# Optimization experiments

Hardware: AMD Instinct MI355X
Metric: run time of the kernel (lower is better)

## Reference

```python
import jax, jax.numpy as jnp
import numpy as np

B, S, D, H = 2, 2048, 1024, 16
HD = D // H  # head_dim = 64


def setup_inputs() -> dict:
    key = jax.random.key(0)
    ks = jax.random.split(key, 11)
    init = 1.0 / np.sqrt(D)
    inp = {
        "query": jax.random.normal(ks[0], (B, S, D), jnp.float32),
        "key": jax.random.normal(ks[1], (B, S, D), jnp.float32),
        "value": jax.random.normal(ks[2], (B, S, D), jnp.float32),
        "Wq": jax.random.uniform(ks[3], (D, D), jnp.float32, -init, init),
        "bq": jax.random.uniform(ks[4], (D,), jnp.float32, -init, init),
        "Wk": jax.random.uniform(ks[5], (D, D), jnp.float32, -init, init),
        "bk": jax.random.uniform(ks[6], (D,), jnp.float32, -init, init),
        "Wv": jax.random.uniform(ks[7], (D, D), jnp.float32, -init, init),
        "bv": jax.random.uniform(ks[8], (D,), jnp.float32, -init, init),
        "Wo": jax.random.uniform(ks[9], (D, D), jnp.float32, -init, init),
        "bo": jax.random.uniform(ks[10], (D,), jnp.float32, -init, init),
    }
    return inp


def reference(query, key, value, Wq, bq, Wk, bk, Wv, bv, Wo, bo):
    # Linear projections (torch Linear: x @ W.T + b)
    q = query @ Wq.T + bq  # [B,S,D]
    k = key @ Wk.T + bk
    v = value @ Wv.T + bv
    # split heads -> [B,H,S,HD]
    q = q.reshape(B, S, H, HD).transpose(0, 2, 1, 3)
    k = k.reshape(B, S, H, HD).transpose(0, 2, 1, 3)
    v = v.reshape(B, S, H, HD).transpose(0, 2, 1, 3)
    # NOTE: original code divides by scale = head_dim**-0.5, i.e. multiplies
    # scores by sqrt(head_dim). Reproduced faithfully.
    scale = HD ** (-0.5)
    scores = jnp.einsum("bhqd,bhkd->bhqk", q, k) / scale  # [B,H,S,S]
    attn = jax.nn.softmax(scores, axis=-1)
    x = jnp.einsum("bhqk,bhkd->bhqd", attn, v)  # [B,H,S,HD]
    x = x.transpose(0, 2, 1, 3).reshape(B, S, D)
    return x @ Wo.T + bo
```

## Files before the change

### kernel.cpp

```cpp
#include <hip/hip_runtime.h>
#include <stdint.h>
#include <stddef.h>

#define SCALE_LOG2E 11.541560327111707f
#define E8 4194304
#define M1 1048576
#define NROW 65536

typedef __attribute__((ext_vector_type(8))) _Float16 f16x8;
typedef __attribute__((ext_vector_type(4))) _Float16 f16x4;
typedef __attribute__((ext_vector_type(4))) float f32x4;

#if __has_builtin(__builtin_amdgcn_exp2f)
#define EXP2F(x) __builtin_amdgcn_exp2f(x)
#else
#define EXP2F(x) exp2f(x)
#endif

__device__ __forceinline__ f32x4 mfma_f16(f16x8 a, f16x8 b, f32x4 c) {
  return __builtin_amdgcn_mfma_f32_16x16x32_f16(a, b, c, 0, 0, 0);
}

__device__ __forceinline__ f32x4 mfma16_f16(f16x4 a, f16x4 b, f32x4 c) {
  return __builtin_amdgcn_mfma_f32_16x16x16f16(a, b, c, 0, 0, 0);
}

__device__ __forceinline__ void async16(const void* g, void* lds) {
  __builtin_amdgcn_global_load_lds(
      (const __attribute__((address_space(1))) unsigned int*)g,
      (__attribute__((address_space(3))) unsigned int*)lds, 16, 0, 0);
}

__global__ void prep_all(const float* __restrict__ q, const float* __restrict__ k,
                         const float* __restrict__ v,
                         const float* __restrict__ wq, const float* __restrict__ wk,
                         const float* __restrict__ wv, const float* __restrict__ wo,
                         _Float16* __restrict__ Xf, _Float16* __restrict__ Wf) {
  const int gid = blockIdx.x;
  const float* src;
  _Float16* dst;
  int i;
  if (gid < 12288) {
    const int z = gid >> 12;
    src = (z == 0) ? q : (z == 1) ? k : v;
    dst = Xf + (size_t)z * E8;
    i = (gid & 4095) * 256 + threadIdx.x;
  } else {
    const int g2 = gid - 12288;
    const int z = g2 >> 10;
    src = (z == 0) ? wq : (z == 1) ? wk : (z == 2) ? wv : wo;
    dst = Wf + (size_t)z * M1;
    i = (g2 & 1023) * 256 + threadIdx.x;
  }
  float4 x = ((const float4*)src)[i];
  f16x4 h = {(_Float16)x.x, (_Float16)x.y, (_Float16)x.z, (_Float16)x.w};
  ((f16x4*)dst)[i] = h;
}

__global__ __launch_bounds__(256, 3) void gemm_qkv(
    const _Float16* __restrict__ Xf,
    const _Float16* __restrict__ Wf,
    const float* __restrict__ bq, const float* __restrict__ bk,
    const float* __restrict__ bv,
    _Float16* __restrict__ Of)
{
  __shared__ _Float16 SMEM[16384];
  _Float16* LA = SMEM;
  _Float16* LB = SMEM + 8192;
  const int z = blockIdx.z;
  const int tid = threadIdx.x;
  const int lane = tid & 63;
  const int wv = tid >> 6;
  const int wm = wv >> 1, wn = wv & 1;
  const int rl = lane & 15, qd = lane >> 4;
  const int m0 = blockIdx.y * 128, n0 = blockIdx.x * 128;

  const _Float16* A0 = Xf + (size_t)z * E8;
  const _Float16* W0 = Wf + (size_t)z * M1;
  const float* bias = (z == 0) ? bq : (z == 1) ? bk : bv;

  f32x4 acc[4][4];
#pragma unroll
  for (int i = 0; i < 4; i++)
#pragma unroll
    for (int j = 0; j < 4; j++) acc[i][j] = f32x4{0.f, 0.f, 0.f, 0.f};

  const int srow = wv * 32 + (lane >> 2);
  const int scol = (lane & 3) * 8;

  auto stage = [&](int k0, int buf) {
    const _Float16* ga = A0 + (size_t)(m0 + srow) * 1024 + k0 + scol;
    async16(ga, &LA[buf * 4096 + wv * 1024]);
    async16(ga + 16 * 1024, &LA[buf * 4096 + wv * 1024 + 512]);
    const _Float16* gb = W0 + (size_t)(n0 + srow) * 1024 + k0 + scol;
    async16(gb, &LB[buf * 4096 + wv * 1024]);
    async16(gb + 16 * 1024, &LB[buf * 4096 + wv * 1024 + 512]);
  };

  stage(0, 0);
  for (int t = 0; t < 32; t++) {
    const int buf = t & 1;
    __syncthreads();
    if (t + 1 < 32) stage((t + 1) * 32, buf ^ 1);
    f16x8 af[4], bfr[4];
#pragma unroll
    for (int i = 0; i < 4; i++) af[i] = *(const f16x8*)&LA[buf * 4096 + (wm * 64 + i * 16 + rl) * 32 + qd * 8];
#pragma unroll
    for (int j = 0; j < 4; j++) bfr[j] = *(const f16x8*)&LB[buf * 4096 + (wn * 64 + j * 16 + rl) * 32 + qd * 8];
#pragma unroll
    for (int i = 0; i < 4; i++)
#pragma unroll
      for (int j = 0; j < 4; j++) acc[i][j] = mfma_f16(af[i], bfr[j], acc[i][j]);
  }

  if (z == 2) {
#pragma unroll
    for (int j = 0; j < 4; j++) {
      const int nn = n0 + wn * 64 + j * 16 + rl;
      const float bj = bias[nn];
      const int hh = nn >> 6, e = nn & 63;
#pragma unroll
      for (int i = 0; i < 4; i++) {
        const int mm = m0 + wm * 64 + i * 16 + qd * 4;
        const int b = mm >> 11, s = mm & 2047;
        f16x4 pk = {(_Float16)(acc[i][j][0] + bj), (_Float16)(acc[i][j][1] + bj),
                    (_Float16)(acc[i][j][2] + bj), (_Float16)(acc[i][j][3] + bj)};
        *(f16x4*)(Of + 2 * (size_t)E8 + (((size_t)((b * 16 + hh) * 64 + e)) << 11) + s) = pk;
      }
    }
  } else {
    const float scl = (z == 0) ? SCALE_LOG2E : 1.0f;
    _Float16* base = Of + (size_t)z * E8;
    __syncthreads();
#pragma unroll
    for (int j = 0; j < 4; j++) {
      const int nl = wn * 64 + j * 16 + rl;
      const float bj = bias[n0 + nl];
#pragma unroll
      for (int i = 0; i < 4; i++) {
        const int ml = wm * 64 + i * 16 + qd * 4;
        const int np = nl ^ (qd << 4);
#pragma unroll
        for (int r = 0; r < 4; r++)
          SMEM[(ml + r) * 128 + np] = (_Float16)((acc[i][j][r] + bj) * scl);
      }
    }
    __syncthreads();
#pragma unroll
    for (int it2 = 0; it2 < 8; it2++) {
      const int m = (it2 * 256 + tid) >> 4;
      const int col8 = (tid & 15) * 8;
      const int np = col8 ^ (((m >> 2) & 3) << 4);
      f16x8 vrow = *(const f16x8*)&SMEM[m * 128 + np];
      const int sg = m0 + m;
      const int b = sg >> 11, s = sg & 2047;
      const int nn = n0 + col8;
      const int hh = nn >> 6, e = nn & 63;
      *(f16x8*)(base + (((size_t)((b * 16 + hh) * 2048 + s)) << 6) + e) = vrow;
    }
  }
}

__global__ __launch_bounds__(256, 4) void attn_kernel(
    const _Float16* __restrict__ Qb,
    const _Float16* __restrict__ Kb,
    const _Float16* __restrict__ Vt,
    float* __restrict__ Op,
    float2* __restrict__ ML)
{
  __shared__ _Float16 Ks[2][4096];
  __shared__ _Float16 Vs[2][4096];
  const int tid = threadIdx.x;
  const int lane = tid & 63;
  const int wv = tid >> 6;
  const int rl = lane & 15, qd = lane >> 4;
  const int bh = blockIdx.z;
  const int half = blockIdx.y;
  const int kvb = half * 1024;
  const int q0 = blockIdx.x * 128 + wv * 32;

  f16x8 qf[2][2];
#pragma unroll
  for (int mt = 0; mt < 2; mt++)
#pragma unroll
    for (int kk = 0; kk < 2; kk++)
      qf[mt][kk] = *(const f16x8*)(Qb + ((size_t)bh * 2048 + q0 + mt * 16 + rl) * 64 +
                                   kk * 32 + qd * 8);

  float m_[2] = {-1e30f, -1e30f}, l_[2] = {0.f, 0.f};
  f32x4 o[2][4];
#pragma unroll
  for (int mt = 0; mt < 2; mt++)
#pragma unroll
    for (int jt = 0; jt < 4; jt++) o[mt][jt] = f32x4{0.f, 0.f, 0.f, 0.f};

  auto stage = [&](int kv, int buf) {
#pragma unroll
    for (int it = 0; it < 2; it++) {
      const int cI = it * 256 + tid;
      const int row = cI >> 3;
      const int c = (cI & 7) ^ (row & 7);
      const int dst = (it * 256 + wv * 64) * 8;
      async16(Kb + ((size_t)bh * 2048 + kv + row) * 64 + c * 8, &Ks[buf][dst]);
      async16(Vt + ((size_t)bh * 64 + row) * 2048 + kv + c * 8, &Vs[buf][dst]);
    }
  };

  stage(kvb, 0);

  for (int t = 0; t < 16; t++) {
    const int buf = t & 1;
    __syncthreads();
    if (t + 1 < 16) stage(kvb + (t + 1) * 64, buf ^ 1);

    f32x4 sc[2][4];
#pragma unroll
    for (int mt = 0; mt < 2; mt++)
#pragma unroll
      for (int nt = 0; nt < 4; nt++) sc[mt][nt] = f32x4{0.f, 0.f, 0.f, 0.f};
    __builtin_amdgcn_s_setprio(1);
#pragma unroll
    for (int nt = 0; nt < 4; nt++) {
      const int ro = (nt * 16 + rl) * 64;
#pragma unroll
      for (int kk = 0; kk < 2; kk++) {
        const int cc = (((kk * 4 + qd) ^ (rl & 7)) << 3);
        f16x8 kh = *(const f16x8*)&Ks[buf][ro + cc];
#pragma unroll
        for (int mt = 0; mt < 2; mt++)
          sc[mt][nt] = mfma_f16(kh, qf[mt][kk], sc[mt][nt]);
      }
    }
    __builtin_amdgcn_s_setprio(0);

    f16x4 pf[2][4];
#pragma unroll
    for (int mt = 0; mt < 2; mt++) {
      float a0 = fmaxf(fmaxf(sc[mt][0][0], sc[mt][0][1]), fmaxf(sc[mt][0][2], sc[mt][0][3]));
      float a1 = fmaxf(fmaxf(sc[mt][1][0], sc[mt][1][1]), fmaxf(sc[mt][1][2], sc[mt][1][3]));
      float a2 = fmaxf(fmaxf(sc[mt][2][0], sc[mt][2][1]), fmaxf(sc[mt][2][2], sc[mt][2][3]));
      float a3 = fmaxf(fmaxf(sc[mt][3][0], sc[mt][3][1]), fmaxf(sc[mt][3][2], sc[mt][3][3]));
      float mloc = fmaxf(fmaxf(a0, a1), fmaxf(a2, a3));
      float mx = fmaxf(mloc, __shfl_xor(mloc, 16));
      mx = fmaxf(mx, __shfl_xor(mx, 32));
      const float mold = m_[mt];
      float mnew = mold;
      if (__any(mx > mold + 8.f)) {
        mnew = fmaxf(mold, mx);
        const float al = EXP2F(mold - mnew);
        l_[mt] *= al;
#pragma unroll
        for (int jt = 0; jt < 4; jt++)
#pragma unroll
          for (int r = 0; r < 4; r++) o[mt][jt][r] *= al;
        m_[mt] = mnew;
      }
      float sm = 0.f;
#pragma unroll
      for (int nt = 0; nt < 4; nt++) {
        const float p0 = EXP2F(sc[mt][nt][0] - mnew);
        const float p1 = EXP2F(sc[mt][nt][1] - mnew);
        const float p2 = EXP2F(sc[mt][nt][2] - mnew);
        const float p3 = EXP2F(sc[mt][nt][3] - mnew);
        sm += (p0 + p1) + (p2 + p3);
        pf[mt][nt] = f16x4{(_Float16)p0, (_Float16)p1, (_Float16)p2, (_Float16)p3};
      }
      l_[mt] += sm;
    }

    __builtin_amdgcn_s_setprio(1);
#pragma unroll
    for (int nt = 0; nt < 4; nt++) {
      const int cb = nt * 2 + (qd >> 1);
#pragma unroll
      for (int jt = 0; jt < 4; jt++) {
        const int row = jt * 16 + rl;
        f16x4 vvv = *(const f16x4*)&Vs[buf][row * 64 + ((cb ^ (rl & 7)) << 3) + (qd & 1) * 4];
        o[0][jt] = mfma16_f16(vvv, pf[0][nt], o[0][jt]);
        o[1][jt] = mfma16_f16(vvv, pf[1][nt], o[1][jt]);
      }
    }
    __builtin_amdgcn_s_setprio(0);
  }

#pragma unroll
  for (int mt = 0; mt < 2; mt++) {
    float lt = l_[mt] + __shfl_xor(l_[mt], 16);
    lt += __shfl_xor(lt, 32);
    const size_t row = (size_t)bh * 2048 + q0 + mt * 16 + rl;
    float* op = Op + ((size_t)half * NROW + row) * 64;
#pragma unroll
    for (int jt = 0; jt < 4; jt++)
      *(f32x4*)(op + jt * 16 + qd * 4) = o[mt][jt];
    if (qd == 0) ML[(size_t)half * NROW + row] = make_float2(m_[mt], lt);
  }
}

__global__ void merge_kernel(const float* __restrict__ Op,
                             const float2* __restrict__ ML,
                             _Float16* __restrict__ Xo) {
  const int t = threadIdx.x;
  const int row = blockIdx.x * 16 + (t >> 4);
  const int d0 = (t & 15) * 4;
  const float2 ml1 = ML[row];
  const float2 ml2 = ML[NROW + row];
  const float m = fmaxf(ml1.x, ml2.x);
  const float w1 = EXP2F(ml1.x - m), w2 = EXP2F(ml2.x - m);
  const float inv = 1.0f / (ml1.y * w1 + ml2.y * w2);
  const float4 o1 = *(const float4*)(Op + (size_t)row * 64 + d0);
  const float4 o2 = *(const float4*)(Op + (size_t)NROW * 64 + (size_t)row * 64 + d0);
  const int bh = row >> 11, q = row & 2047;
  const int b = bh >> 4, hh = bh & 15;
  f16x4 pk = {(_Float16)((o1.x * w1 + o2.x * w2) * inv),
              (_Float16)((o1.y * w1 + o2.y * w2) * inv),
              (_Float16)((o1.z * w1 + o2.z * w2) * inv),
              (_Float16)((o1.w * w1 + o2.w * w2) * inv)};
  *(f16x4*)(Xo + ((size_t)(b * 2048 + q)) * 1024 + hh * 64 + d0) = pk;
}

__global__ __launch_bounds__(256, 2) void gemm_out(
    const _Float16* __restrict__ A0,
    const _Float16* __restrict__ W0,
    const float* __restrict__ bias,
    float* __restrict__ out)
{
  __shared__ _Float16 LA[2][2048];
  __shared__ _Float16 LB[2][4096];
  const int tid = threadIdx.x;
  const int lane = tid & 63;
  const int wv = tid >> 6;
  const int wm = wv >> 1, wn = wv & 1;
  const int rl = lane & 15, qd = lane >> 4;
  const int m0 = blockIdx.y * 64, n0 = blockIdx.x * 128;

  f32x4 acc[2][4];
#pragma unroll
  for (int i = 0; i < 2; i++)
#pragma unroll
    for (int j = 0; j < 4; j++) acc[i][j] = f32x4{0.f, 0.f, 0.f, 0.f};

  auto stage = [&](int k0, int buf) {
    {
      const int row = tid >> 2, c = tid & 3;
      async16(A0 + (size_t)(m0 + row) * 1024 + k0 + c * 8, &LA[buf][wv * 512]);
    }
#pragma unroll
    for (int it = 0; it < 2; it++) {
      const int cI = it * 256 + tid;
      const int row = cI >> 2, c = cI & 3;
      async16(W0 + (size_t)(n0 + row) * 1024 + k0 + c * 8,
              &LB[buf][it * 2048 + wv * 512]);
    }
  };

  stage(0, 0);
  for (int t = 0; t < 32; t++) {
    const int buf = t & 1;
    __syncthreads();
    if (t + 1 < 32) stage((t + 1) * 32, buf ^ 1);
    f16x8 af[2], bfr[4];
#pragma unroll
    for (int i = 0; i < 2; i++) af[i] = *(const f16x8*)&LA[buf][(wm * 32 + i * 16 + rl) * 32 + qd * 8];
#pragma unroll
    for (int j = 0; j < 4; j++) bfr[j] = *(const f16x8*)&LB[buf][(wn * 64 + j * 16 + rl) * 32 + qd * 8];
#pragma unroll
    for (int i = 0; i < 2; i++)
#pragma unroll
      for (int j = 0; j < 4; j++) acc[i][j] = mfma_f16(af[i], bfr[j], acc[i][j]);
  }

#pragma unroll
  for (int j = 0; j < 4; j++) {
    const int nn = n0 + wn * 64 + j * 16 + rl;
    const float bj = bias[nn];
#pragma unroll
    for (int i = 0; i < 2; i++) {
      const int mm = m0 + wm * 32 + i * 16 + qd * 4;
#pragma unroll
      for (int r = 0; r < 4; r++)
        out[(size_t)(mm + r) * 1024 + nn] = acc[i][j][r] + bj;
    }
  }
}

extern "C" void kernel_launch(void* const* d_in, const int* in_sizes, int n_in,
                              void* d_out, int out_size, void* d_ws, size_t ws_size,
                              hipStream_t stream) {
  const float* query = (const float*)d_in[0];
  const float* key   = (const float*)d_in[1];
  const float* value = (const float*)d_in[2];
  const float* Wq = (const float*)d_in[3];
  const float* bq = (const float*)d_in[4];
  const float* Wk = (const float*)d_in[5];
  const float* bk = (const float*)d_in[6];
  const float* Wv = (const float*)d_in[7];
  const float* bv = (const float*)d_in[8];
  const float* Wo = (const float*)d_in[9];
  const float* bo = (const float*)d_in[10];

  _Float16* ws = (_Float16*)d_ws;
  _Float16* Xf = ws;
  _Float16* Wf = ws + 3 * (size_t)E8;
  _Float16* Qh = Wf + 4 * (size_t)M1;
  _Float16* Kh = Qh + (size_t)E8;
  _Float16* Vt = Kh + (size_t)E8;
  _Float16* Xa = Vt + (size_t)E8;
  float*    Op = (float*)(Xa + (size_t)E8);
  float2*   ML = (float2*)(Op + 2 * (size_t)NROW * 64);

  prep_all<<<16384, 256, 0, stream>>>(query, key, value, Wq, Wk, Wv, Wo, Xf, Wf);
  gemm_qkv<<<dim3(8, 32, 3), 256, 0, stream>>>(Xf, Wf, bq, bk, bv, Qh);
  attn_kernel<<<dim3(16, 2, 32), 256, 0, stream>>>(Qh, Kh, Vt, Op, ML);
  merge_kernel<<<4096, 256, 0, stream>>>(Op, ML, Xa);
  gemm_out<<<dim3(8, 64), 256, 0, stream>>>(Xa, Wf + 3 * (size_t)M1, bo, (float*)d_out);
}
```

Measured before the change: 249.8 us.

## Stage V through registers with half-swapped swizzle to avoid LDS bank conflicts

V tiles are no longer copied into LDS with async global-to-LDS loads. Each thread now loads V into registers early, then writes it to LDS after the PV MFMA loop. On write, odd-indexed waves (wv&1, which map to rows with bit 3 set) swap the two 4-element halves of each 16-byte chunk, and the PV read adds a matching XOR on the half offset. This is meant to remove LDS bank conflicts on the 4-wide V fragment reads. The cost is extra VGPRs held across the loop and a changed barrier placement, which could hurt occupancy at 4 waves/SIMD.

```diff
diff --git a/kernel.cpp b/kernel.cpp
--- a/kernel.cpp
+++ b/kernel.cpp
@@ -174,10 +174,12 @@
   const int lane = tid & 63;
   const int wv = tid >> 6;
   const int rl = lane & 15, qd = lane >> 4;
+  const int rl3 = (rl >> 3) & 1;
   const int bh = blockIdx.z;
   const int half = blockIdx.y;
   const int kvb = half * 1024;
   const int q0 = blockIdx.x * 128 + wv * 32;
+  const int swp = __builtin_amdgcn_readfirstlane(wv & 1);
 
   f16x8 qf[2][2];
 #pragma unroll
@@ -194,24 +196,48 @@
 #pragma unroll
     for (int jt = 0; jt < 4; jt++) o[mt][jt] = f32x4{0.f, 0.f, 0.f, 0.f};
 
-  auto stage = [&](int kv, int buf) {
+  auto stageK = [&](int kv, int buf) {
 #pragma unroll
     for (int it = 0; it < 2; it++) {
       const int cI = it * 256 + tid;
       const int row = cI >> 3;
       const int c = (cI & 7) ^ (row & 7);
-      const int dst = (it * 256 + wv * 64) * 8;
-      async16(Kb + ((size_t)bh * 2048 + kv + row) * 64 + c * 8, &Ks[buf][dst]);
-      async16(Vt + ((size_t)bh * 64 + row) * 2048 + kv + c * 8, &Vs[buf][dst]);
+      async16(Kb + ((size_t)bh * 2048 + kv + row) * 64 + c * 8,
+              &Ks[buf][(it * 256 + wv * 64) * 8]);
     }
   };
-
-  stage(kvb, 0);
+  auto loadV = [&](int kv, f16x8* g) {
+#pragma unroll
+    for (int it = 0; it < 2; it++) {
+      const int cI = it * 256 + tid;
+      const int row = cI >> 3;
+      g[it] = *(const f16x8*)(Vt + ((size_t)bh * 64 + row) * 2048 + kv + (cI & 7) * 8);
+    }
+  };
+  auto writeV = [&](int buf, const f16x8* g) {
+#pragma unroll
+    for (int it = 0; it < 2; it++) {
+      const int cI = it * 256 + tid;
+      const int row = cI >> 3;
+      const int C = (cI & 7) ^ (row & 7);
+      f16x8 w = g[it];
+      if (swp) w = __builtin_shufflevector(w, w, 4, 5, 6, 7, 0, 1, 2, 3);
+      *(f16x8*)&Vs[buf][row * 64 + C * 8] = w;
+    }
+  };
+
+  f16x8 vg[2];
+  stageK(kvb, 0);
+  loadV(kvb, vg);
+  writeV(0, vg);
+  __syncthreads();
 
   for (int t = 0; t < 16; t++) {
     const int buf = t & 1;
-    __syncthreads();
-    if (t + 1 < 16) stage(kvb + (t + 1) * 64, buf ^ 1);
+    if (t + 1 < 16) {
+      loadV(kvb + (t + 1) * 64, vg);
+      stageK(kvb + (t + 1) * 64, buf ^ 1);
+    }
 
     f32x4 sc[2][4];
 #pragma unroll
@@ -269,18 +295,21 @@
     }
 
     __builtin_amdgcn_s_setprio(1);
+    const int pbit = ((qd & 1) ^ rl3) << 2;
 #pragma unroll
     for (int nt = 0; nt < 4; nt++) {
-      const int cb = nt * 2 + (qd >> 1);
+      const int cpart = (((nt * 2 + (qd >> 1)) ^ (rl & 7)) << 3);
 #pragma unroll
       for (int jt = 0; jt < 4; jt++) {
-        const int row = jt * 16 + rl;
-        f16x4 vvv = *(const f16x4*)&Vs[buf][row * 64 + ((cb ^ (rl & 7)) << 3) + (qd & 1) * 4];
+        f16x4 vvv = *(const f16x4*)&Vs[buf][(jt * 16 + rl) * 64 + cpart + pbit];
         o[0][jt] = mfma16_f16(vvv, pf[0][nt], o[0][jt]);
         o[1][jt] = mfma16_f16(vvv, pf[1][nt], o[1][jt]);
       }
     }
     __builtin_amdgcn_s_setprio(0);
+
+    if (t + 1 < 16) writeV(buf ^ 1, vg);
+    __syncthreads();
   }
 
 #pragma unroll
```

Result: no change. 252.0 us (+0.9%).

## Shrink attention tiles to 16 query rows per wave and 32-key blocks

Applied to the files above, without the earlier changes.

The attention kernel now gives each wave 16 query rows instead of 32 and processes 32-key tiles instead of 64. The grid doubles and launch bounds target 8 blocks per CU. V is no longer copied asynchronously; it is loaded into registers and written to a re-swizzled LDS layout after the compute, with one barrier per iteration. This trades K/V reuse per block (twice the LDS and global traffic per query) for higher occupancy and lower register pressure.

```diff
diff --git a/kernel.cpp b/kernel.cpp
--- a/kernel.cpp
+++ b/kernel.cpp
@@ -161,15 +161,15 @@
   }
 }
 
-__global__ __launch_bounds__(256, 4) void attn_kernel(
+__global__ __launch_bounds__(256, 8) void attn_kernel(
     const _Float16* __restrict__ Qb,
     const _Float16* __restrict__ Kb,
     const _Float16* __restrict__ Vt,
     float* __restrict__ Op,
     float2* __restrict__ ML)
 {
-  __shared__ _Float16 Ks[2][4096];
-  __shared__ _Float16 Vs[2][4096];
+  __shared__ _Float16 Ks[2][2048];
+  __shared__ _Float16 Vs[2][2048];
   const int tid = threadIdx.x;
   const int lane = tid & 63;
   const int wv = tid >> 6;
@@ -177,122 +177,121 @@
   const int bh = blockIdx.z;
   const int half = blockIdx.y;
   const int kvb = half * 1024;
-  const int q0 = blockIdx.x * 128 + wv * 32;
-
-  f16x8 qf[2][2];
-#pragma unroll
-  for (int mt = 0; mt < 2; mt++)
-#pragma unroll
-    for (int kk = 0; kk < 2; kk++)
-      qf[mt][kk] = *(const f16x8*)(Qb + ((size_t)bh * 2048 + q0 + mt * 16 + rl) * 64 +
-                                   kk * 32 + qd * 8);
-
-  float m_[2] = {-1e30f, -1e30f}, l_[2] = {0.f, 0.f};
-  f32x4 o[2][4];
-#pragma unroll
-  for (int mt = 0; mt < 2; mt++)
-#pragma unroll
-    for (int jt = 0; jt < 4; jt++) o[mt][jt] = f32x4{0.f, 0.f, 0.f, 0.f};
-
-  auto stage = [&](int kv, int buf) {
-#pragma unroll
-    for (int it = 0; it < 2; it++) {
-      const int cI = it * 256 + tid;
-      const int row = cI >> 3;
-      const int c = (cI & 7) ^ (row & 7);
-      const int dst = (it * 256 + wv * 64) * 8;
-      async16(Kb + ((size_t)bh * 2048 + kv + row) * 64 + c * 8, &Ks[buf][dst]);
-      async16(Vt + ((size_t)bh * 64 + row) * 2048 + kv + c * 8, &Vs[buf][dst]);
-    }
+  const int q0 = blockIdx.x * 64 + wv * 16;
+
+  f16x8 qf[2];
+#pragma unroll
+  for (int kk = 0; kk < 2; kk++)
+    qf[kk] = *(const f16x8*)(Qb + ((size_t)bh * 2048 + q0 + rl) * 64 + kk * 32 + qd * 8);
+
+  float m_ = -1e30f, l_ = 0.f;
+  f32x4 o[4];
+#pragma unroll
+  for (int jt = 0; jt < 4; jt++) o[jt] = f32x4{0.f, 0.f, 0.f, 0.f};
+
+  auto stageK = [&](int kv, int buf) {
+    const int row = tid >> 3;
+    const int c = (tid & 7) ^ (row & 7);
+    async16(Kb + ((size_t)bh * 2048 + kv + row) * 64 + c * 8, &Ks[buf][wv * 512]);
   };
-
-  stage(kvb, 0);
-
-  for (int t = 0; t < 16; t++) {
+  auto loadV = [&](int kv, f16x8& g) {
+    const int row = tid >> 2;
+    g = *(const f16x8*)(Vt + ((size_t)bh * 64 + row) * 2048 + kv + (tid & 3) * 8);
+  };
+  auto writeV = [&](int buf, f16x8 g) {
+    const int row = tid >> 2;
+    const int cpos = (tid & 3) ^ ((row >> 2) & 3);
+    f16x8 w = (row & 2) ? __builtin_shufflevector(g, g, 4, 5, 6, 7, 0, 1, 2, 3) : g;
+    *(f16x8*)&Vs[buf][row * 32 + cpos * 8] = w;
+  };
+
+  f16x8 vg;
+  stageK(kvb, 0);
+  loadV(kvb, vg);
+  writeV(0, vg);
+  __syncthreads();
+
+  for (int t = 0; t < 32; t++) {
     const int buf = t & 1;
-    __syncthreads();
-    if (t + 1 < 16) stage(kvb + (t + 1) * 64, buf ^ 1);
-
-    f32x4 sc[2][4];
-#pragma unroll
-    for (int mt = 0; mt < 2; mt++)
-#pragma unroll
-      for (int nt = 0; nt < 4; nt++) sc[mt][nt] = f32x4{0.f, 0.f, 0.f, 0.f};
+    if (t + 1 < 32) {
+      loadV(kvb + (t + 1) * 32, vg);
+      stageK(kvb + (t + 1) * 32, buf ^ 1);
+    }
+
+    f32x4 sc[2];
+#pragma unroll
+    for (int nt = 0; nt < 2; nt++) sc[nt] = f32x4{0.f, 0.f, 0.f, 0.f};
     __builtin_amdgcn_s_setprio(1);
 #pragma unroll
-    for (int nt = 0; nt < 4; nt++) {
+    for (int nt = 0; nt < 2; nt++) {
       const int ro = (nt * 16 + rl) * 64;
 #pragma unroll
       for (int kk = 0; kk < 2; kk++) {
         const int cc = (((kk * 4 + qd) ^ (rl & 7)) << 3);
         f16x8 kh = *(const f16x8*)&Ks[buf][ro + cc];
-#pragma unroll
-        for (int mt = 0; mt < 2; mt++)
-          sc[mt][nt] = mfma_f16(kh, qf[mt][kk], sc[mt][nt]);
+        sc[nt] = mfma_f16(kh, qf[kk], sc[nt]);
       }
     }
     __builtin_amdgcn_s_setprio(0);
 
-    f16x4 pf[2][4];
-#pragma unroll
-    for (int mt = 0; mt < 2; mt++) {
-      float a0 = fmaxf(fmaxf(sc[mt][0][0], sc[mt][0][1]), fmaxf(sc[mt][0][2], sc[mt][0][3]));
-      float a1 = fmaxf(fmaxf(sc[mt][1][0], sc[mt][1][1]), fmaxf(sc[mt][1][2], sc[mt][1][3]));
-      float a2 = fmaxf(fmaxf(sc[mt][2][0], sc[mt][2][1]), fmaxf(sc[mt][2][2], sc[mt][2][3]));
-      float a3 = fmaxf(fmaxf(sc[mt][3][0], sc[mt][3][1]), fmaxf(sc[mt][3][2], sc[mt][3][3]));
-      float mloc = fmaxf(fmaxf(a0, a1), fmaxf(a2, a3));
+    f16x4 pf[2];
+    {
+      float a0 = fmaxf(fmaxf(sc[0][0], sc[0][1]), fmaxf(sc[0][2], sc[0][3]));
+      float a1 = fmaxf(fmaxf(sc[1][0], sc[1][1]), fmaxf(sc[1][2], sc[1][3]));
+      float mloc = fmaxf(a0, a1);
       float mx = fmaxf(mloc, __shfl_xor(mloc, 16));
       mx = fmaxf(mx, __shfl_xor(mx, 32));
-      const float mold = m_[mt];
+      const float mold = m_;
       float mnew = mold;
       if (__any(mx > mold + 8.f)) {
         mnew = fmaxf(mold, mx);
         const float al = EXP2F(mold - mnew);
-        l_[mt] *= al;
+        l_ *= al;
 #pragma unroll
         for (int jt = 0; jt < 4; jt++)
 #pragma unroll
-          for (int r = 0; r < 4; r++) o[mt][jt][r] *= al;
-        m_[mt] = mnew;
+          for (int r = 0; r < 4; r++) o[jt][r] *= al;
+        m_ = mnew;
       }
       float sm = 0.f;
 #pragma unroll
-      for (int nt = 0; nt < 4; nt++) {
-        const float p0 = EXP2F(sc[mt][nt][0] - mnew);
-        const float p1 = EXP2F(sc[mt][nt][1] - mnew);
-        const float p2 = EXP2F(sc[mt][nt][2] - mnew);
-        const float p3 = EXP2F(sc[mt][nt][3] - mnew);
+      for (int nt = 0; nt < 2; nt++) {
+        const float p0 = EXP2F(sc[nt][0] - mnew);
+        const float p1 = EXP2F(sc[nt][1] - mnew);
+        const float p2 = EXP2F(sc[nt][2] - mnew);
+        const float p3 = EXP2F(sc[nt][3] - mnew);
         sm += (p0 + p1) + (p2 + p3);
-        pf[mt][nt] = f16x4{(_Float16)p0, (_Float16)p1, (_Float16)p2, (_Float16)p3};
-      }
-      l_[mt] += sm;
+        pf[nt] = f16x4{(_Float16)p0, (_Float16)p1, (_Float16)p2, (_Float16)p3};
+      }
+      l_ += sm;
     }
 
     __builtin_amdgcn_s_setprio(1);
-#pragma unroll
-    for (int nt = 0; nt < 4; nt++) {
-      const int cb = nt * 2 + (qd >> 1);
+    const int rg = (rl >> 1) & 7;
+#pragma unroll
+    for (int nt = 0; nt < 2; nt++) {
+      const int sl = ((nt * 4 + qd) ^ rg) << 2;
 #pragma unroll
       for (int jt = 0; jt < 4; jt++) {
-        const int row = jt * 16 + rl;
-        f16x4 vvv = *(const f16x4*)&Vs[buf][row * 64 + ((cb ^ (rl & 7)) << 3) + (qd & 1) * 4];
-        o[0][jt] = mfma16_f16(vvv, pf[0][nt], o[0][jt]);
-        o[1][jt] = mfma16_f16(vvv, pf[1][nt], o[1][jt]);
+        f16x4 vvv = *(const f16x4*)&Vs[buf][(jt * 16 + rl) * 32 + sl];
+        o[jt] = mfma16_f16(vvv, pf[nt], o[jt]);
       }
     }
     __builtin_amdgcn_s_setprio(0);
-  }
-
-#pragma unroll
-  for (int mt = 0; mt < 2; mt++) {
-    float lt = l_[mt] + __shfl_xor(l_[mt], 16);
+
+    if (t + 1 < 32) writeV(buf ^ 1, vg);
+    __syncthreads();
+  }
+
+  {
+    float lt = l_ + __shfl_xor(l_, 16);
     lt += __shfl_xor(lt, 32);
-    const size_t row = (size_t)bh * 2048 + q0 + mt * 16 + rl;
+    const size_t row = (size_t)bh * 2048 + q0 + rl;
     float* op = Op + ((size_t)half * NROW + row) * 64;
 #pragma unroll
     for (int jt = 0; jt < 4; jt++)
-      *(f32x4*)(op + jt * 16 + qd * 4) = o[mt][jt];
-    if (qd == 0) ML[(size_t)half * NROW + row] = make_float2(m_[mt], lt);
+      *(f32x4*)(op + jt * 16 + qd * 4) = o[jt];
+    if (qd == 0) ML[(size_t)half * NROW + row] = make_float2(m_, lt);
   }
 }
 
@@ -410,7 +409,7 @@
 
   prep_all<<<16384, 256, 0, stream>>>(query, key, value, Wq, Wk, Wv, Wo, Xf, Wf);
   gemm_qkv<<<dim3(8, 32, 3), 256, 0, stream>>>(Xf, Wf, bq, bk, bv, Qh);
-  attn_kernel<<<dim3(16, 2, 32), 256, 0, stream>>>(Qh, Kh, Vt, Op, ML);
+  attn_kernel<<<dim3(32, 2, 32), 256, 0, stream>>>(Qh, Kh, Vt, Op, ML);
   merge_kernel<<<4096, 256, 0, stream>>>(Op, ML, Xa);
   gemm_out<<<dim3(8, 64), 256, 0, stream>>>(Xa, Wf + 3 * (size_t)M1, bo, (float*)d_out);
 }
```

Measured after the change: 248.5 us. Within noise of the previous version (-0.5%).
